# Kernel tuning notes

Measured on AMD Instinct MI355X. Metric: run time of the kernel, lower is better.

Reference implementation:

```python
import jax, jax.numpy as jnp
import numpy as np

N = 100000   # nodes
C = 128      # channels
K = 16       # clusters
E = 3200000  # edges (avg degree 32)


def setup_inputs() -> dict:
    key = jax.random.key(0)
    k1, k2, k3, k4 = jax.random.split(key, 4)
    features = jax.random.normal(k1, (N, C), dtype=jnp.float32)
    edge_row = jax.random.randint(k2, (E,), 0, N, dtype=jnp.int32)
    edge_col = jax.random.randint(k3, (E,), 0, N, dtype=jnp.int32)
    edge_val = jnp.ones((E,), dtype=jnp.float32)
    # orthogonal-ish init for fc weight (matches nn.init.orthogonal_ in spirit)
    w = jax.random.normal(k4, (K, C), dtype=jnp.float32)
    q, _ = jnp.linalg.qr(w.T)          # [C, K], orthonormal columns
    fc_w = q.T.astype(jnp.float32)     # [K, C]
    fc_b = jnp.zeros((K,), dtype=jnp.float32)
    return {"features": features, "edge_row": edge_row, "edge_col": edge_col,
            "edge_val": edge_val, "fc_w": fc_w, "fc_b": fc_b}


def reference(features, edge_row, edge_col, edge_val, fc_w, fc_b):
    collapse_regularization = 1.0
    n_nodes = features.shape[0]
    n_clusters = fc_w.shape[0]

    # assignments = softmax(Linear(features))  -> [N, K]
    assignments = jax.nn.softmax(features @ fc_w.T + fc_b, axis=1)
    cluster_sizes = jnp.sum(assignments, axis=0)            # [K]
    assignments_pooling = assignments / cluster_sizes       # [N, K]

    # degrees = column sums of sparse adjacency (no densification)
    degrees = jax.ops.segment_sum(edge_val, edge_col, num_segments=n_nodes)  # [N]
    number_of_edges = jnp.sum(degrees)

    # sparse A @ assignments via segment_sum over edges -> [N, K]
    a_s = jax.ops.segment_sum(edge_val[:, None] * assignments[edge_col],
                              edge_row, num_segments=n_nodes)
    graph_pooled = a_s.T @ assignments                      # S^T A S, [K, K]

    normalizer_left = assignments.T @ degrees[:, None]      # [K, 1]
    normalizer_right = degrees[None, :] @ assignments       # [1, K]
    normalizer = (normalizer_left @ normalizer_right) / 2.0 / number_of_edges

    spectral_loss = -jnp.trace(graph_pooled - normalizer) / 2.0 / number_of_edges
    sk = np.sqrt(n_clusters).astype(np.float32)
    collapse_loss = (jnp.sum(jnp.abs(cluster_sizes - n_nodes / n_clusters))
                     / n_nodes * sk / (sk - 1.0) / 2.0)
    loss = spectral_loss + collapse_regularization * collapse_loss

    features_pooled = jax.nn.selu(assignments_pooling.T @ features)  # [K, C]
    features_pooled = assignments_pooling @ features_pooled          # unpool [N, C]
    return features_pooled, assignments, loss
```

## Files before the change

### kernel.cpp

```cpp
#include <hip/hip_runtime.h>
#include <hip/hip_fp16.h>
#include <math.h>


#define WS_ESUM 0
#define WS_TR   1
#define WS_M    2
#define WS_CS   18
#define WS_B    64
#define WS_P2   2112

#define OFF_AH  0
#define OFF_CSP 800000
#define OFF_EP  825008
#define OFF_BP  861872

__global__ __launch_bounds__(256) void k_assign(
    const float* __restrict__ F, const float* __restrict__ W,
    const float* __restrict__ bias, float* __restrict__ A,
    __half* __restrict__ Ah, float* __restrict__ csp, int N) {
  __shared__ float Ws[2048];
  __shared__ float csred[4][16];
  int t = threadIdx.x;
#pragma unroll
  for (int i = 0; i < 8; i++) Ws[t + 256 * i] = W[t + 256 * i];
  __syncthreads();

  int p = t & 3;
  int nl = t >> 2;
  int n = blockIdx.x * 64 + nl;
  bool active = (n < N);

  float a[16];
#pragma unroll
  for (int k = 0; k < 16; k++) a[k] = 0.f;

  if (active) {
    const float4* f4 = (const float4*)(F + (size_t)n * 128 + p * 32);
#pragma unroll
    for (int i = 0; i < 8; i++) {
      float4 f = f4[i];
#pragma unroll
      for (int k = 0; k < 16; k++) {
        float4 w = *(const float4*)(&Ws[k * 128 + p * 32 + i * 4]);
        a[k] = fmaf(f.x, w.x, a[k]);
        a[k] = fmaf(f.y, w.y, a[k]);
        a[k] = fmaf(f.z, w.z, a[k]);
        a[k] = fmaf(f.w, w.w, a[k]);
      }
    }
  }

#pragma unroll
  for (int k = 0; k < 16; k++) {
    a[k] += __shfl_xor(a[k], 1, 64);
    a[k] += __shfl_xor(a[k], 2, 64);
  }

#pragma unroll
  for (int k = 0; k < 16; k++) a[k] += bias[k];
  float mx = a[0];
#pragma unroll
  for (int k = 1; k < 16; k++) mx = fmaxf(mx, a[k]);
  float s = 0.f;
#pragma unroll
  for (int k = 0; k < 16; k++) { a[k] = __expf(a[k] - mx); s += a[k]; }
  float inv = 1.0f / s;
#pragma unroll
  for (int k = 0; k < 16; k++) a[k] *= inv;

  if (active) {
    float4 g = make_float4(a[p * 4 + 0], a[p * 4 + 1], a[p * 4 + 2], a[p * 4 + 3]);
    ((float4*)(A + (size_t)n * 16))[p] = g;
    if (p == 0) {
      __half2 hh[4];
      hh[0].x = __float2half_rn(a[0]); hh[0].y = __float2half_rn(a[1]);
      hh[1].x = __float2half_rn(a[2]); hh[1].y = __float2half_rn(a[3]);
      hh[2].x = __float2half_rn(a[4]); hh[2].y = __float2half_rn(a[5]);
      hh[3].x = __float2half_rn(a[6]); hh[3].y = __float2half_rn(a[7]);
      *(uint4*)(Ah + (size_t)n * 16) = *(uint4*)hh;
    } else if (p == 1) {
      __half2 hh[4];
      hh[0].x = __float2half_rn(a[8]);  hh[0].y = __float2half_rn(a[9]);
      hh[1].x = __float2half_rn(a[10]); hh[1].y = __float2half_rn(a[11]);
      hh[2].x = __float2half_rn(a[12]); hh[2].y = __float2half_rn(a[13]);
      hh[3].x = __float2half_rn(a[14]); hh[3].y = __float2half_rn(a[15]);
      *(uint4*)(Ah + (size_t)n * 16 + 8) = *(uint4*)hh;
    }
  }

  int lane = t & 63, wid = t >> 6;
#pragma unroll
  for (int k = 0; k < 16; k++) {
    float v = (active && p == 0) ? a[k] : 0.f;
    for (int off = 32; off; off >>= 1) v += __shfl_xor(v, off, 64);
    if (lane == 0) csred[wid][k] = v;
  }
  __syncthreads();
  if (t < 16)
    csp[(size_t)blockIdx.x * 16 + t] =
        csred[0][t] + csred[1][t] + csred[2][t] + csred[3][t];
}

union H2F4 { float4 f4; __half2 h2[4]; };

__device__ __forceinline__ void edge_body(
    const __half* __restrict__ Ah, int r, int c, float v,
    float& eS, float& tr, float* m) {
  const float4* pc = (const float4*)(Ah + (size_t)c * 16);
  const float4* pr = (const float4*)(Ah + (size_t)r * 16);
  H2F4 uc0, uc1, ur0, ur1;
  uc0.f4 = pc[0]; uc1.f4 = pc[1];
  ur0.f4 = pr[0]; ur1.f4 = pr[1];
  float cf[16], rf[16];
#pragma unroll
  for (int j = 0; j < 4; j++) {
    float2 f;
    f = __half22float2(uc0.h2[j]); cf[2 * j] = f.x; cf[2 * j + 1] = f.y;
    f = __half22float2(uc1.h2[j]); cf[8 + 2 * j] = f.x; cf[9 + 2 * j] = f.y;
    f = __half22float2(ur0.h2[j]); rf[2 * j] = f.x; rf[2 * j + 1] = f.y;
    f = __half22float2(ur1.h2[j]); rf[8 + 2 * j] = f.x; rf[9 + 2 * j] = f.y;
  }
  eS += v;
  float d = 0.f;
#pragma unroll
  for (int k = 0; k < 16; k++) {
    m[k] = fmaf(v, cf[k], m[k]);
    d = fmaf(rf[k], cf[k], d);
  }
  tr = fmaf(v, d, tr);
}

__global__ __launch_bounds__(256) void k_edge(
    const int* __restrict__ row, const int* __restrict__ col,
    const float* __restrict__ val, const __half* __restrict__ Ah,
    float* __restrict__ ep, int E) {
  float eS = 0.f, tr = 0.f;
  float m[16];
#pragma unroll
  for (int i = 0; i < 16; i++) m[i] = 0.f;

  int tid = blockIdx.x * 256 + threadIdx.x;
  int T = gridDim.x * 256;
  int e = tid;
  for (; e + T < E; e += 2 * T) {
    int r0 = row[e], c0 = col[e];
    int r1 = row[e + T], c1 = col[e + T];
    float v0 = val[e], v1 = val[e + T];
    edge_body(Ah, r0, c0, v0, eS, tr, m);
    edge_body(Ah, r1, c1, v1, eS, tr, m);
  }
  for (; e < E; e += T)
    edge_body(Ah, row[e], col[e], val[e], eS, tr, m);

  float vals[18];
  vals[0] = eS; vals[1] = tr;
#pragma unroll
  for (int i = 0; i < 16; i++) vals[2 + i] = m[i];
#pragma unroll
  for (int i = 0; i < 18; i++) {
    float v = vals[i];
    for (int off = 32; off; off >>= 1) v += __shfl_xor(v, off, 64);
    vals[i] = v;
  }
  __shared__ float red[4][18];
  int lane = threadIdx.x & 63, wid = threadIdx.x >> 6;
  if (lane == 0) {
#pragma unroll
    for (int i = 0; i < 18; i++) red[wid][i] = vals[i];
  }
  __syncthreads();
  if (threadIdx.x < 18)
    ep[(size_t)blockIdx.x * 18 + threadIdx.x] =
        red[0][threadIdx.x] + red[1][threadIdx.x] +
        red[2][threadIdx.x] + red[3][threadIdx.x];
}

__global__ __launch_bounds__(256) void k_nodeB(
    const float* __restrict__ F, const float* __restrict__ A,
    float* __restrict__ bp, int N) {
  int t = threadIdx.x;
  int q = t & 31;
  int sub = t >> 5;

  float4 acc[16];
#pragma unroll
  for (int k = 0; k < 16; k++) acc[k] = make_float4(0.f, 0.f, 0.f, 0.f);

  const float4* F4 = (const float4*)F;
  const float4* A4 = (const float4*)A;
  int stride = gridDim.x * 8;
  for (int n = blockIdx.x * 8 + sub; n < N; n += stride) {
    float4 f  = F4[(size_t)n * 32 + q];
    float4 a0 = A4[(size_t)n * 4 + 0];
    float4 a1 = A4[(size_t)n * 4 + 1];
    float4 a2 = A4[(size_t)n * 4 + 2];
    float4 a3 = A4[(size_t)n * 4 + 3];
    float av[16] = {a0.x, a0.y, a0.z, a0.w, a1.x, a1.y, a1.z, a1.w,
                    a2.x, a2.y, a2.z, a2.w, a3.x, a3.y, a3.z, a3.w};
#pragma unroll
    for (int k = 0; k < 16; k++) {
      acc[k].x = fmaf(av[k], f.x, acc[k].x);
      acc[k].y = fmaf(av[k], f.y, acc[k].y);
      acc[k].z = fmaf(av[k], f.z, acc[k].z);
      acc[k].w = fmaf(av[k], f.w, acc[k].w);
    }
  }

#pragma unroll
  for (int k = 0; k < 16; k++) {
    acc[k].x += __shfl_xor(acc[k].x, 32, 64);
    acc[k].y += __shfl_xor(acc[k].y, 32, 64);
    acc[k].z += __shfl_xor(acc[k].z, 32, 64);
    acc[k].w += __shfl_xor(acc[k].w, 32, 64);
  }

  __shared__ float red[4][2048];
  int lane = t & 63, wid = t >> 6;
  if (lane < 32) {
#pragma unroll
    for (int k = 0; k < 16; k++)
      *(float4*)&red[wid][k * 128 + q * 4] = acc[k];
  }
  __syncthreads();
  float* myp = bp + (size_t)blockIdx.x * 2048;
#pragma unroll
  for (int qq = 0; qq < 2; qq++) {
    int base = t * 8 + qq * 4;
    float4 s0 = *(float4*)&red[0][base];
    float4 s1 = *(float4*)&red[1][base];
    float4 s2 = *(float4*)&red[2][base];
    float4 s3 = *(float4*)&red[3][base];
    *(float4*)&myp[base] = make_float4(s0.x + s1.x + s2.x + s3.x,
                                       s0.y + s1.y + s2.y + s3.y,
                                       s0.z + s1.z + s2.z + s3.z,
                                       s0.w + s1.w + s2.w + s3.w);
  }
}

__global__ __launch_bounds__(256) void k_reduce(
    const float* __restrict__ csp, const float* __restrict__ ep,
    const float* __restrict__ bp, float* __restrict__ ws,
    int GA, int GE, int GB) {
  __shared__ float L[256];
  int t = threadIdx.x;
  int b = blockIdx.x;
  if (b < 256) {
    int cell = b * 8 + (t & 7);
    int seg = t >> 3;
    float s0 = 0.f, s1 = 0.f, s2 = 0.f, s3 = 0.f;
    int g = seg;
    for (; g + 96 < GB; g += 128) {
      s0 += bp[(size_t)g * 2048 + cell];
      s1 += bp[(size_t)(g + 32) * 2048 + cell];
      s2 += bp[(size_t)(g + 64) * 2048 + cell];
      s3 += bp[(size_t)(g + 96) * 2048 + cell];
    }
    for (; g < GB; g += 32) s0 += bp[(size_t)g * 2048 + cell];
    L[t] = (s0 + s1) + (s2 + s3);
    __syncthreads();
    if (t < 8) {
      float tot = 0.f;
#pragma unroll
      for (int s = 0; s < 32; s++) tot += L[s * 8 + t];
      ws[WS_B + b * 8 + t] = tot;
    }
  } else if (b == 256) {
    int n = GE * 18;
    float s0 = 0.f, s1 = 0.f, s2 = 0.f, s3 = 0.f;
    if (t < 252) {
      int f = t;
      for (; f + 756 < n; f += 1008) {
        s0 += ep[f]; s1 += ep[f + 252]; s2 += ep[f + 504]; s3 += ep[f + 756];
      }
      for (; f < n; f += 252) s0 += ep[f];
    }
    L[t] = (s0 + s1) + (s2 + s3);
    __syncthreads();
    if (t < 18) {
      float tot = 0.f;
#pragma unroll
      for (int j = 0; j < 14; j++) tot += L[j * 18 + t];
      ws[t] = tot;
    }
  } else {
    int n = GA * 16;
    float s0 = 0.f, s1 = 0.f, s2 = 0.f, s3 = 0.f;
    int f = t;
    for (; f + 768 < n; f += 1024) {
      s0 += csp[f]; s1 += csp[f + 256]; s2 += csp[f + 512]; s3 += csp[f + 768];
    }
    for (; f < n; f += 256) s0 += csp[f];
    L[t] = (s0 + s1) + (s2 + s3);
    __syncthreads();
    if (t < 16) {
      float tot = 0.f;
#pragma unroll
      for (int j = 0; j < 16; j++) tot += L[j * 16 + t];
      ws[WS_CS + t] = tot;
    }
  }
}

__global__ __launch_bounds__(256) void k_finalize(
    float* __restrict__ ws, float* __restrict__ loss_out, int N) {
  __shared__ float invcs[16];
  int t = threadIdx.x;
  if (t < 16) invcs[t] = 1.0f / ws[WS_CS + t];
  __syncthreads();
  const float* B = ws + WS_B;
  float* P2 = ws + WS_P2;
  const float scale = 1.0507009873554805f;
  const float alpha = 1.6732632423543772f;
#pragma unroll
  for (int idx = t; idx < 2048; idx += 256) {
    int k = idx >> 7;
    float x = B[idx] * invcs[k];
    float s = (x > 0.f) ? scale * x : scale * alpha * expm1f(x);
    P2[idx] = s * invcs[k];
  }
  if (t == 0) {
    float Es = ws[WS_ESUM], tr = ws[WS_TR];
    float m2 = 0.f;
#pragma unroll
    for (int i = 0; i < 16; i++) m2 += ws[WS_M + i] * ws[WS_M + i];
    float spectral = -(tr - m2 / (2.0f * Es)) / (2.0f * Es);
    float coll = 0.f;
    float tgt = (float)N / 16.0f;
#pragma unroll
    for (int i = 0; i < 16; i++) coll += fabsf(ws[WS_CS + i] - tgt);
    coll = coll / (float)N * (4.0f / 3.0f / 2.0f);
    loss_out[0] = spectral + coll;
  }
}

__global__ __launch_bounds__(256) void k_unpool(
    const float* __restrict__ A, const float* __restrict__ P2,
    float* __restrict__ out, int N) {
  __shared__ float Ps[2048];
  int t = threadIdx.x;
#pragma unroll
  for (int i = 0; i < 8; i++) Ps[t + 256 * i] = P2[t + 256 * i];
  __syncthreads();
  int c = t & 127;
  int half = t >> 7;
  int pairs = (N + 1) >> 1;
  for (int p = blockIdx.x; p < pairs; p += gridDim.x) {
    int n = p * 2 + half;
    if (n < N) {
      const float4* a4 = (const float4*)(A + (size_t)n * 16);
      float4 a0 = a4[0], a1 = a4[1], a2 = a4[2], a3 = a4[3];
      float s = a0.x * Ps[0 * 128 + c] + a0.y * Ps[1 * 128 + c]
              + a0.z * Ps[2 * 128 + c] + a0.w * Ps[3 * 128 + c]
              + a1.x * Ps[4 * 128 + c] + a1.y * Ps[5 * 128 + c]
              + a1.z * Ps[6 * 128 + c] + a1.w * Ps[7 * 128 + c]
              + a2.x * Ps[8 * 128 + c] + a2.y * Ps[9 * 128 + c]
              + a2.z * Ps[10 * 128 + c] + a2.w * Ps[11 * 128 + c]
              + a3.x * Ps[12 * 128 + c] + a3.y * Ps[13 * 128 + c]
              + a3.z * Ps[14 * 128 + c] + a3.w * Ps[15 * 128 + c];
      out[(size_t)n * 128 + c] = s;
    }
  }
}

extern "C" void kernel_launch(void* const* d_in, const int* in_sizes, int n_in,
                              void* d_out, int out_size, void* d_ws, size_t ws_size,
                              hipStream_t stream) {
  const float* F    = (const float*)d_in[0];
  const int*   erow = (const int*)d_in[1];
  const int*   ecol = (const int*)d_in[2];
  const float* eval_= (const float*)d_in[3];
  const float* W    = (const float*)d_in[4];
  const float* bias = (const float*)d_in[5];

  int N = in_sizes[0] / 128;
  int E = in_sizes[1];

  float* out0 = (float*)d_out;
  float* A    = out0 + (size_t)N * 128;
  float* loss = A + (size_t)N * 16;
  float* ws   = (float*)d_ws;

  int GA = (N + 63) / 64;
  int GE = 2048;
  int GB = 1024;

  __half* Ah  = (__half*)(out0 + OFF_AH);
  float*  csp = out0 + OFF_CSP;
  float*  ep  = out0 + OFF_EP;
  float*  bp  = out0 + OFF_BP;

  k_assign<<<GA, 256, 0, stream>>>(F, W, bias, A, Ah, csp, N);
  k_edge<<<GE, 256, 0, stream>>>(erow, ecol, eval_, Ah, ep, E);
  k_nodeB<<<GB, 256, 0, stream>>>(F, A, bp, N);
  k_reduce<<<258, 256, 0, stream>>>(csp, ep, bp, ws, GA, GE, GB);
  k_finalize<<<1, 256, 0, stream>>>(ws, loss, N);
  k_unpool<<<1024, 256, 0, stream>>>(A, ws + WS_P2, out0, N);
}
```

Before: 269.6 us.

## Batch edge gathers by four, two nodes per thread, vectorize unpool stores

Three kernels change. The edge kernel now gives each thread four consecutive edges, loads their indices with vector nontemporal loads, and issues all eight Ah gathers before computing, to raise memory-level parallelism; the edge grid becomes 1563 blocks. The assign kernel handles two nodes per thread with a padded shared-memory weight layout to cut bank conflicts and reuse each weight load. The unpool kernel keeps P2 columns in registers and writes float4 outputs instead of scalar stores, at the cost of more registers per thread.

```diff
diff --git a/kernel.cpp b/kernel.cpp
--- a/kernel.cpp
+++ b/kernel.cpp
@@ -15,84 +15,125 @@
 #define OFF_EP  825008
 #define OFF_BP  861872
 
+typedef int   int4v   __attribute__((ext_vector_type(4)));
+typedef float float4v __attribute__((ext_vector_type(4)));
+
 __global__ __launch_bounds__(256) void k_assign(
     const float* __restrict__ F, const float* __restrict__ W,
     const float* __restrict__ bias, float* __restrict__ A,
     __half* __restrict__ Ah, float* __restrict__ csp, int N) {
-  __shared__ float Ws[2048];
+  __shared__ float Ws[16 * 144];
   __shared__ float csred[4][16];
   int t = threadIdx.x;
 #pragma unroll
-  for (int i = 0; i < 8; i++) Ws[t + 256 * i] = W[t + 256 * i];
+  for (int i = 0; i < 8; i++) {
+    int idx = t + 256 * i;
+    int k = idx >> 7, r = idx & 127;
+    Ws[k * 144 + (r >> 5) * 36 + (r & 31)] = W[idx];
+  }
   __syncthreads();
 
   int p = t & 3;
-  int nl = t >> 2;
-  int n = blockIdx.x * 64 + nl;
-  bool active = (n < N);
-
-  float a[16];
-#pragma unroll
-  for (int k = 0; k < 16; k++) a[k] = 0.f;
-
-  if (active) {
-    const float4* f4 = (const float4*)(F + (size_t)n * 128 + p * 32);
-#pragma unroll
-    for (int i = 0; i < 8; i++) {
-      float4 f = f4[i];
-#pragma unroll
-      for (int k = 0; k < 16; k++) {
-        float4 w = *(const float4*)(&Ws[k * 128 + p * 32 + i * 4]);
-        a[k] = fmaf(f.x, w.x, a[k]);
-        a[k] = fmaf(f.y, w.y, a[k]);
-        a[k] = fmaf(f.z, w.z, a[k]);
-        a[k] = fmaf(f.w, w.w, a[k]);
-      }
+  int slot = t >> 2;
+  int n0 = blockIdx.x * 128 + slot;
+  int n1 = n0 + 64;
+  bool act0 = (n0 < N), act1 = (n1 < N);
+  int n0c = act0 ? n0 : (N - 1);
+  int n1c = act1 ? n1 : (N - 1);
+
+  float a0[16], a1[16];
+#pragma unroll
+  for (int k = 0; k < 16; k++) { a0[k] = 0.f; a1[k] = 0.f; }
+
+  const float4* f0 = (const float4*)(F + (size_t)n0c * 128 + p * 32);
+  const float4* f1 = (const float4*)(F + (size_t)n1c * 128 + p * 32);
+#pragma unroll
+  for (int i = 0; i < 8; i++) {
+    float4 x0 = f0[i];
+    float4 x1 = f1[i];
+#pragma unroll
+    for (int k = 0; k < 16; k++) {
+      float4 w = *(const float4*)(&Ws[k * 144 + p * 36 + i * 4]);
+      a0[k] = fmaf(x0.x, w.x, a0[k]);
+      a0[k] = fmaf(x0.y, w.y, a0[k]);
+      a0[k] = fmaf(x0.z, w.z, a0[k]);
+      a0[k] = fmaf(x0.w, w.w, a0[k]);
+      a1[k] = fmaf(x1.x, w.x, a1[k]);
+      a1[k] = fmaf(x1.y, w.y, a1[k]);
+      a1[k] = fmaf(x1.z, w.z, a1[k]);
+      a1[k] = fmaf(x1.w, w.w, a1[k]);
     }
   }
 
 #pragma unroll
   for (int k = 0; k < 16; k++) {
-    a[k] += __shfl_xor(a[k], 1, 64);
-    a[k] += __shfl_xor(a[k], 2, 64);
-  }
-
-#pragma unroll
-  for (int k = 0; k < 16; k++) a[k] += bias[k];
-  float mx = a[0];
-#pragma unroll
-  for (int k = 1; k < 16; k++) mx = fmaxf(mx, a[k]);
-  float s = 0.f;
-#pragma unroll
-  for (int k = 0; k < 16; k++) { a[k] = __expf(a[k] - mx); s += a[k]; }
-  float inv = 1.0f / s;
-#pragma unroll
-  for (int k = 0; k < 16; k++) a[k] *= inv;
-
-  if (active) {
-    float4 g = make_float4(a[p * 4 + 0], a[p * 4 + 1], a[p * 4 + 2], a[p * 4 + 3]);
-    ((float4*)(A + (size_t)n * 16))[p] = g;
+    a0[k] += __shfl_xor(a0[k], 1, 64);
+    a0[k] += __shfl_xor(a0[k], 2, 64);
+    a1[k] += __shfl_xor(a1[k], 1, 64);
+    a1[k] += __shfl_xor(a1[k], 2, 64);
+  }
+
+#pragma unroll
+  for (int k = 0; k < 16; k++) { a0[k] += bias[k]; a1[k] += bias[k]; }
+
+  float mx0 = a0[0], mx1 = a1[0];
+#pragma unroll
+  for (int k = 1; k < 16; k++) { mx0 = fmaxf(mx0, a0[k]); mx1 = fmaxf(mx1, a1[k]); }
+  float s0 = 0.f, s1 = 0.f;
+#pragma unroll
+  for (int k = 0; k < 16; k++) {
+    a0[k] = __expf(a0[k] - mx0); s0 += a0[k];
+    a1[k] = __expf(a1[k] - mx1); s1 += a1[k];
+  }
+  float inv0 = 1.0f / s0, inv1 = 1.0f / s1;
+#pragma unroll
+  for (int k = 0; k < 16; k++) { a0[k] *= inv0; a1[k] *= inv1; }
+
+  if (act0)
+    ((float4*)(A + (size_t)n0 * 16))[p] =
+        make_float4(a0[p * 4 + 0], a0[p * 4 + 1], a0[p * 4 + 2], a0[p * 4 + 3]);
+  if (act1)
+    ((float4*)(A + (size_t)n1 * 16))[p] =
+        make_float4(a1[p * 4 + 0], a1[p * 4 + 1], a1[p * 4 + 2], a1[p * 4 + 3]);
+
+  if (p == 0 && act0) {
+    __half2 hh[4];
+    hh[0].x = __float2half_rn(a0[0]); hh[0].y = __float2half_rn(a0[1]);
+    hh[1].x = __float2half_rn(a0[2]); hh[1].y = __float2half_rn(a0[3]);
+    hh[2].x = __float2half_rn(a0[4]); hh[2].y = __float2half_rn(a0[5]);
+    hh[3].x = __float2half_rn(a0[6]); hh[3].y = __float2half_rn(a0[7]);
+    *(uint4*)(Ah + (size_t)n0 * 16) = *(uint4*)hh;
+  } else if (p == 1 && act0) {
+    __half2 hh[4];
+    hh[0].x = __float2half_rn(a0[8]);  hh[0].y = __float2half_rn(a0[9]);
+    hh[1].x = __float2half_rn(a0[10]); hh[1].y = __float2half_rn(a0[11]);
+    hh[2].x = __float2half_rn(a0[12]); hh[2].y = __float2half_rn(a0[13]);
+    hh[3].x = __float2half_rn(a0[14]); hh[3].y = __float2half_rn(a0[15]);
+    *(uint4*)(Ah + (size_t)n0 * 16 + 8) = *(uint4*)hh;
+  } else if (p == 2 && act1) {
+    __half2 hh[4];
+    hh[0].x = __float2half_rn(a1[0]); hh[0].y = __float2half_rn(a1[1]);
+    hh[1].x = __float2half_rn(a1[2]); hh[1].y = __float2half_rn(a1[3]);
+    hh[2].x = __float2half_rn(a1[4]); hh[2].y = __float2half_rn(a1[5]);
+    hh[3].x = __float2half_rn(a1[6]); hh[3].y = __float2half_rn(a1[7]);
+    *(uint4*)(Ah + (size_t)n1 * 16) = *(uint4*)hh;
+  } else if (p == 3 && act1) {
+    __half2 hh[4];
+    hh[0].x = __float2half_rn(a1[8]);  hh[0].y = __float2half_rn(a1[9]);
+    hh[1].x = __float2half_rn(a1[10]); hh[1].y = __float2half_rn(a1[11]);
+    hh[2].x = __float2half_rn(a1[12]); hh[2].y = __float2half_rn(a1[13]);
+    hh[3].x = __float2half_rn(a1[14]); hh[3].y = __float2half_rn(a1[15]);
+    *(uint4*)(Ah + (size_t)n1 * 16 + 8) = *(uint4*)hh;
+  }
+
+  int lane = t & 63, wid = t >> 6;
+#pragma unroll
+  for (int k = 0; k < 16; k++) {
+    float v = 0.f;
     if (p == 0) {
-      __half2 hh[4];
-      hh[0].x = __float2half_rn(a[0]); hh[0].y = __float2half_rn(a[1]);
-      hh[1].x = __float2half_rn(a[2]); hh[1].y = __float2half_rn(a[3]);
-      hh[2].x = __float2half_rn(a[4]); hh[2].y = __float2half_rn(a[5]);
-      hh[3].x = __float2half_rn(a[6]); hh[3].y = __float2half_rn(a[7]);
-      *(uint4*)(Ah + (size_t)n * 16) = *(uint4*)hh;
-    } else if (p == 1) {
-      __half2 hh[4];
-      hh[0].x = __float2half_rn(a[8]);  hh[0].y = __float2half_rn(a[9]);
-      hh[1].x = __float2half_rn(a[10]); hh[1].y = __float2half_rn(a[11]);
-      hh[2].x = __float2half_rn(a[12]); hh[2].y = __float2half_rn(a[13]);
-      hh[3].x = __float2half_rn(a[14]); hh[3].y = __float2half_rn(a[15]);
-      *(uint4*)(Ah + (size_t)n * 16 + 8) = *(uint4*)hh;
-    }
-  }
-
-  int lane = t & 63, wid = t >> 6;
-#pragma unroll
-  for (int k = 0; k < 16; k++) {
-    float v = (active && p == 0) ? a[k] : 0.f;
+      if (act0) v += a0[k];
+      if (act1) v += a1[k];
+    }
     for (int off = 32; off; off >>= 1) v += __shfl_xor(v, off, 64);
     if (lane == 0) csred[wid][k] = v;
   }
@@ -131,6 +172,46 @@
   tr = fmaf(v, d, tr);
 }
 
+__device__ __forceinline__ void group4(
+    const __half* __restrict__ Ah, const int* __restrict__ row,
+    const int* __restrict__ col, const float* __restrict__ val, int e,
+    float& eS, float& tr, float* m) {
+  int4v   ri = __builtin_nontemporal_load((const int4v*)(row + e));
+  int4v   ci = __builtin_nontemporal_load((const int4v*)(col + e));
+  float4v vi = __builtin_nontemporal_load((const float4v*)(val + e));
+
+  H2F4 CA[4][2], RA[4][2];
+#pragma unroll
+  for (int j = 0; j < 4; j++) {
+    const float4* pc = (const float4*)(Ah + (size_t)ci[j] * 16);
+    const float4* pr = (const float4*)(Ah + (size_t)ri[j] * 16);
+    CA[j][0].f4 = pc[0]; CA[j][1].f4 = pc[1];
+    RA[j][0].f4 = pr[0]; RA[j][1].f4 = pr[1];
+  }
+
+#pragma unroll
+  for (int j = 0; j < 4; j++) {
+    float vj = vi[j];
+    float cf[16], rf[16];
+#pragma unroll
+    for (int q = 0; q < 4; q++) {
+      float2 f;
+      f = __half22float2(CA[j][0].h2[q]); cf[2 * q] = f.x; cf[2 * q + 1] = f.y;
+      f = __half22float2(CA[j][1].h2[q]); cf[8 + 2 * q] = f.x; cf[9 + 2 * q] = f.y;
+      f = __half22float2(RA[j][0].h2[q]); rf[2 * q] = f.x; rf[2 * q + 1] = f.y;
+      f = __half22float2(RA[j][1].h2[q]); rf[8 + 2 * q] = f.x; rf[9 + 2 * q] = f.y;
+    }
+    eS += vj;
+    float d = 0.f;
+#pragma unroll
+    for (int k = 0; k < 16; k++) {
+      m[k] = fmaf(vj, cf[k], m[k]);
+      d = fmaf(rf[k], cf[k], d);
+    }
+    tr = fmaf(vj, d, tr);
+  }
+}
+
 __global__ __launch_bounds__(256) void k_edge(
     const int* __restrict__ row, const int* __restrict__ col,
     const float* __restrict__ val, const __half* __restrict__ Ah,
@@ -140,18 +221,13 @@
 #pragma unroll
   for (int i = 0; i < 16; i++) m[i] = 0.f;
 
-  int tid = blockIdx.x * 256 + threadIdx.x;
-  int T = gridDim.x * 256;
-  int e = tid;
-  for (; e + T < E; e += 2 * T) {
-    int r0 = row[e], c0 = col[e];
-    int r1 = row[e + T], c1 = col[e + T];
-    float v0 = val[e], v1 = val[e + T];
-    edge_body(Ah, r0, c0, v0, eS, tr, m);
-    edge_body(Ah, r1, c1, v1, eS, tr, m);
-  }
-  for (; e < E; e += T)
-    edge_body(Ah, row[e], col[e], val[e], eS, tr, m);
+  int gid = blockIdx.x * 256 + threadIdx.x;
+  int T4 = gridDim.x * 256 * 4;
+  int E4 = E & ~3;
+  for (int e = gid * 4; e < E4; e += T4)
+    group4(Ah, row, col, val, e, eS, tr, m);
+  if (gid < E - E4)
+    edge_body(Ah, row[E4 + gid], col[E4 + gid], val[E4 + gid], eS, tr, m);
 
   float vals[18];
   vals[0] = eS; vals[1] = tr;
@@ -342,24 +418,27 @@
 #pragma unroll
   for (int i = 0; i < 8; i++) Ps[t + 256 * i] = P2[t + 256 * i];
   __syncthreads();
-  int c = t & 127;
-  int half = t >> 7;
-  int pairs = (N + 1) >> 1;
-  for (int p = blockIdx.x; p < pairs; p += gridDim.x) {
-    int n = p * 2 + half;
-    if (n < N) {
-      const float4* a4 = (const float4*)(A + (size_t)n * 16);
-      float4 a0 = a4[0], a1 = a4[1], a2 = a4[2], a3 = a4[3];
-      float s = a0.x * Ps[0 * 128 + c] + a0.y * Ps[1 * 128 + c]
-              + a0.z * Ps[2 * 128 + c] + a0.w * Ps[3 * 128 + c]
-              + a1.x * Ps[4 * 128 + c] + a1.y * Ps[5 * 128 + c]
-              + a1.z * Ps[6 * 128 + c] + a1.w * Ps[7 * 128 + c]
-              + a2.x * Ps[8 * 128 + c] + a2.y * Ps[9 * 128 + c]
-              + a2.z * Ps[10 * 128 + c] + a2.w * Ps[11 * 128 + c]
-              + a3.x * Ps[12 * 128 + c] + a3.y * Ps[13 * 128 + c]
-              + a3.z * Ps[14 * 128 + c] + a3.w * Ps[15 * 128 + c];
-      out[(size_t)n * 128 + c] = s;
-    }
+  int c4 = (t & 31) << 2;
+  int sub = t >> 5;
+  float4 pk[16];
+#pragma unroll
+  for (int k = 0; k < 16; k++) pk[k] = *(const float4*)&Ps[k * 128 + c4];
+
+  int stride = gridDim.x * 8;
+  for (int n = blockIdx.x * 8 + sub; n < N; n += stride) {
+    const float4* a4 = (const float4*)(A + (size_t)n * 16);
+    float4 a0 = a4[0], a1 = a4[1], a2 = a4[2], a3 = a4[3];
+    float av[16] = {a0.x, a0.y, a0.z, a0.w, a1.x, a1.y, a1.z, a1.w,
+                    a2.x, a2.y, a2.z, a2.w, a3.x, a3.y, a3.z, a3.w};
+    float4 s = make_float4(0.f, 0.f, 0.f, 0.f);
+#pragma unroll
+    for (int k = 0; k < 16; k++) {
+      s.x = fmaf(av[k], pk[k].x, s.x);
+      s.y = fmaf(av[k], pk[k].y, s.y);
+      s.z = fmaf(av[k], pk[k].z, s.z);
+      s.w = fmaf(av[k], pk[k].w, s.w);
+    }
+    *(float4*)(out + (size_t)n * 128 + c4) = s;
   }
 }
 
@@ -381,8 +460,8 @@
   float* loss = A + (size_t)N * 16;
   float* ws   = (float*)d_ws;
 
-  int GA = (N + 63) / 64;
-  int GE = 2048;
+  int GA = (N + 127) / 128;
+  int GE = 1563;
   int GB = 1024;
 
   __half* Ah  = (__half*)(out0 + OFF_AH);
@@ -395,5 +474,5 @@
   k_nodeB<<<GB, 256, 0, stream>>>(F, A, bp, N);
   k_reduce<<<258, 256, 0, stream>>>(csp, ep, bp, ws, GA, GE, GB);
   k_finalize<<<1, 256, 0, stream>>>(ws, loss, N);
-  k_unpool<<<1024, 256, 0, stream>>>(A, ws + WS_P2, out0, N);
-}
+  k_unpool<<<1280, 256, 0, stream>>>(A, ws + WS_P2, out0, N);
+}
```

Result: faster. 260.2 us (-3.5%).
